# Kernel tuning notes

Measured on AMD Instinct MI355X. Metric: run time of the kernel, lower is better.

Reference implementation:

```python
import jax, jax.numpy as jnp
import numpy as np

EPS = 1e-7  # K.epsilon()
NUM_ROUTING = 3

def squash(v, axis=-1):
    s = jnp.sum(jnp.square(v), axis=axis, keepdims=True)
    scale = s / (1.0 + s) / jnp.sqrt(s + EPS)
    return scale * v

def setup_inputs() -> dict:
    key = jax.random.key(0)
    k1, k2 = jax.random.split(key)
    B, J, I = 64, 2048, 16   # batch, input_num_capsule, input_dim_capsule
    K_, D = 32, 16           # num_capsule, dim_capsule
    inputs = jax.random.normal(k1, (B, J, I), dtype=jnp.float32)
    W = jax.random.normal(k2, (K_, J, D, I), dtype=jnp.float32) * 0.05
    return {"inputs": inputs, "W": W}

def reference(inputs, W):
    # inputs: [B, J, I]; W: [K, J, D, I]
    # inputs_hat[b,k,j,d] = sum_i inputs[b,j,i] * W[k,j,d,i]
    u_hat = jnp.einsum('bji,kjdi->bkjd', inputs, W)  # [B,K,J,D]
    B, K_, J, D = u_hat.shape
    b = jnp.zeros((B, K_, J), dtype=u_hat.dtype)
    for i in range(NUM_ROUTING):
        c = jax.nn.softmax(b, axis=1)                # softmax over num_capsule (dim=1)
        s = jnp.einsum('bkj,bkjd->bkd', c, u_hat)    # [B,K,D]
        outputs = squash(s)
        if i < NUM_ROUTING - 1:
            b = b + jnp.einsum('bkd,bkjd->bkj', outputs, u_hat)
    return jnp.concatenate([outputs, c], axis=-1)    # [B, K, D+J]
```

## Files before the change

### kernel.cpp

```cpp
#include <hip/hip_runtime.h>
#include <hip/hip_bf16.h>

#define B_ 64
#define J_ 2048
#define K_ 32
#define D_ 16
#define KD 512
#define NCH 256
#define JCR 8

typedef __attribute__((ext_vector_type(8))) short short8v;
typedef __attribute__((ext_vector_type(16))) float f32x16;

__device__ __forceinline__ float bf2f(unsigned int bits16) {
  unsigned int u = bits16 << 16;
  return __builtin_bit_cast(float, u);
}
__device__ __forceinline__ unsigned int f2bf(float f) {
  unsigned int u = __builtin_bit_cast(unsigned int, f);
  u = u + 0x7fffu + ((u >> 16) & 1u);
  return u >> 16;
}
__device__ __forceinline__ unsigned int cvtpk(float lo, float hi) {
  unsigned int r;
  asm("v_cvt_pk_bf16_f32 %0, %1, %2" : "=v"(r) : "v"(lo), "v"(hi));
  return r;
}
__device__ __forceinline__ f32x16 zero16() {
  f32x16 z;
#pragma unroll
  for (int i = 0; i < 16; ++i) z[i] = 0.f;
  return z;
}

__global__ __launch_bounds__(256) void k_prepX(const float* __restrict__ inp,
                                               unsigned short* __restrict__ XT) {
  const size_t tid = (size_t)blockIdx.x * 256 + threadIdx.x;
  const size_t stride = (size_t)gridDim.x * 256;
  for (size_t g8 = tid; g8 < (size_t)J_ * B_ * 2; g8 += stride) {
    const size_t o = g8 * 8;
    const int j = (int)(o >> 10), b = (int)((o >> 4) & 63), i0 = (int)(o & 15);
    const float* src = inp + ((size_t)b * J_ + j) * 16 + i0;
    const float4 a = *(const float4*)src;
    const float4 c = *(const float4*)(src + 4);
    uint4 pk;
    pk.x = cvtpk(a.x, a.y);
    pk.y = cvtpk(a.z, a.w);
    pk.z = cvtpk(c.x, c.y);
    pk.w = cvtpk(c.z, c.w);
    *(uint4*)(XT + o) = pk;
  }
}

__global__ __launch_bounds__(512, 2) void k_R0W(const float* __restrict__ W,
                                                const unsigned short* __restrict__ XT,
                                                unsigned short* __restrict__ WB,
                                                unsigned int* __restrict__ spart_pk) {
  const int ch = blockIdx.x;
  const int t = threadIdx.x;
  const int wave = t >> 6, lane = t & 63;
  const int kq = wave & 3, bt = wave >> 2;
  const int hi = lane >> 5, b31 = lane & 31;
  const int b = bt * 32 + b31;
  const int j0 = ch * JCR;

  const float* wsrc = W + ((size_t)(8 * kq + (b31 >> 4)) * J_ + j0) * 256 +
                      (b31 & 15) * 16 + 8 * hi;
  unsigned short* wdst = WB + (size_t)j0 * 8192 + kq * 2048 + (b31 >> 4) * 256 +
                         (b31 & 15) * 16 + 8 * hi;
  const unsigned short* xBase = XT + (size_t)j0 * 1024 + b * 16 + 8 * hi;
  const size_t qstep = (size_t)2 * J_ * 256;

  f32x16 acc[4];
#pragma unroll
  for (int q = 0; q < 4; ++q) acc[q] = zero16();

  float4 wc[8];
  uint4 xc;
#pragma unroll
  for (int q = 0; q < 4; ++q) {
    wc[2 * q]     = *(const float4*)(wsrc + (size_t)q * qstep);
    wc[2 * q + 1] = *(const float4*)(wsrc + (size_t)q * qstep + 4);
  }
  xc = *(const uint4*)xBase;

  for (int jj = 0; jj < JCR; ++jj) {
    float4 wn[8];
    uint4 xn;
    if (jj + 1 < JCR) {
#pragma unroll
      for (int q = 0; q < 4; ++q) {
        const float* ws2 = wsrc + (size_t)(jj + 1) * 256 + (size_t)q * qstep;
        wn[2 * q] = *(const float4*)ws2;
        wn[2 * q + 1] = *(const float4*)(ws2 + 4);
      }
      xn = *(const uint4*)(xBase + (size_t)(jj + 1) * 1024);
    }
    const short8v xf = __builtin_bit_cast(short8v, xc);
#pragma unroll
    for (int q = 0; q < 4; ++q) {
      uint4 wv;
      wv.x = cvtpk(wc[2 * q].x, wc[2 * q].y);
      wv.y = cvtpk(wc[2 * q].z, wc[2 * q].w);
      wv.z = cvtpk(wc[2 * q + 1].x, wc[2 * q + 1].y);
      wv.w = cvtpk(wc[2 * q + 1].z, wc[2 * q + 1].w);
      if (bt == 0) *(uint4*)(wdst + (size_t)jj * 8192 + q * 512) = wv;
      acc[q] = __builtin_amdgcn_mfma_f32_32x32x16_bf16(
          __builtin_bit_cast(short8v, wv), xf, acc[q], 0, 0, 0);
    }
#pragma unroll
    for (int p = 0; p < 8; ++p) wc[p] = wn[p];
    xc = xn;
  }

  const float sc = 1.f / 32.f;
#pragma unroll
  for (int q = 0; q < 4; ++q) {
    const int keven = 8 * kq + 2 * q;
    unsigned int* se = spart_pk + (((size_t)b * NCH + ch) * 32 + keven) * 8 + 2 * hi;
    *(uint2*)se = make_uint2(cvtpk(acc[q][0] * sc, acc[q][1] * sc),
                             cvtpk(acc[q][2] * sc, acc[q][3] * sc));
    *(uint2*)(se + 4) = make_uint2(cvtpk(acc[q][4] * sc, acc[q][5] * sc),
                                   cvtpk(acc[q][6] * sc, acc[q][7] * sc));
    unsigned int* so = se + 8;
    *(uint2*)so = make_uint2(cvtpk(acc[q][8] * sc, acc[q][9] * sc),
                             cvtpk(acc[q][10] * sc, acc[q][11] * sc));
    *(uint2*)(so + 4) = make_uint2(cvtpk(acc[q][12] * sc, acc[q][13] * sc),
                                   cvtpk(acc[q][14] * sc, acc[q][15] * sc));
  }
}

template <int MODE>
__global__ __launch_bounds__(512, 2) void k_R(const unsigned short* __restrict__ XT,
                                              const unsigned short* __restrict__ WB,
                                              const unsigned short* __restrict__ osB,
                                              unsigned int* __restrict__ spart_pk,
                                              float* __restrict__ outp) {
  const int ch = blockIdx.x;
  const int t = threadIdx.x;
  const int wave = t >> 6, lane = t & 63;
  const int kq = wave & 3, bt = wave >> 2;
  const int hi = lane >> 5, b31 = lane & 31;
  const int b = bt * 32 + b31;
  const int j0 = ch * JCR;

  __shared__ float Sbuf[2 * 4 * 2 * 32];
  __shared__ float c_lds[(MODE == 2) ? 32 * 64 * 9 : 4];

  uint4 os_pk[8];
  {
    const unsigned short* osb = osB + ((size_t)bt * 64 + lane) * 8 + (size_t)(8 * kq) * 1024;
#pragma unroll
    for (int kk = 0; kk < 8; ++kk) os_pk[kk] = *(const uint4*)(osb + (size_t)kk * 1024);
  }

  float acc[4][16];
#pragma unroll
  for (int q = 0; q < 4; ++q)
#pragma unroll
    for (int s = 0; s < 16; ++s) acc[q][s] = 0.f;

  const unsigned short* waBase =
      WB + (size_t)j0 * 8192 + (b31 >> 4) * 256 + (b31 & 15) * 16 + 8 * hi + (size_t)kq * 2048;
  const unsigned short* xBase = XT + (size_t)j0 * 1024 + b * 16 + 8 * hi;

  uint4 a_cur[4], b_cur;
#pragma unroll
  for (int q = 0; q < 4; ++q) a_cur[q] = *(const uint4*)(waBase + q * 512);
  b_cur = *(const uint4*)(xBase);

  for (int jj = 0; jj < JCR; ++jj) {
    uint4 a_nxt[4], b_nxt;
    if (jj + 1 < JCR) {
#pragma unroll
      for (int q = 0; q < 4; ++q)
        a_nxt[q] = *(const uint4*)(waBase + (size_t)(jj + 1) * 8192 + q * 512);
      b_nxt = *(const uint4*)(xBase + (size_t)(jj + 1) * 1024);
    }

    f32x16 u[4];
#pragma unroll
    for (int q = 0; q < 4; ++q)
      u[q] = __builtin_amdgcn_mfma_f32_32x32x16_bf16(
          __builtin_bit_cast(short8v, a_cur[q]), __builtin_bit_cast(short8v, b_cur),
          zero16(), 0, 0, 0);

    float ee[4], eo[4];
    float Sp = 0.f;
#pragma unroll
    for (int q = 0; q < 4; ++q) {
      const unsigned int* o0 = (const unsigned int*)&os_pk[2 * q];
      const unsigned int* o1 = (const unsigned int*)&os_pk[2 * q + 1];
      float pe = 0.f, po = 0.f;
#pragma unroll
      for (int s = 0; s < 8; ++s) {
        const unsigned int w0 = o0[s >> 1], w1 = o1[s >> 1];
        pe = fmaf(u[q][s], bf2f((s & 1) ? (w0 >> 16) : (w0 & 0xffffu)), pe);
        po = fmaf(u[q][8 + s], bf2f((s & 1) ? (w1 >> 16) : (w1 & 0xffffu)), po);
      }
      pe += __shfl_xor(pe, 32);
      po += __shfl_xor(po, 32);
      ee[q] = __expf(pe);
      eo[q] = __expf(po);
      Sp += ee[q] + eo[q];
    }
    if (hi == 0) Sbuf[((jj & 1) * 8 + kq * 2 + bt) * 32 + b31] = Sp;
    __syncthreads();
    const int sb = (jj & 1) * 8;
    const float S = Sbuf[(sb + 0 * 2 + bt) * 32 + b31] + Sbuf[(sb + 1 * 2 + bt) * 32 + b31] +
                    Sbuf[(sb + 2 * 2 + bt) * 32 + b31] + Sbuf[(sb + 3 * 2 + bt) * 32 + b31];
    const float rS = __builtin_amdgcn_rcpf(S);
#pragma unroll
    for (int q = 0; q < 4; ++q) {
      const float ce = ee[q] * rS, co = eo[q] * rS;
#pragma unroll
      for (int s = 0; s < 8; ++s) {
        acc[q][s] = fmaf(ce, u[q][s], acc[q][s]);
        acc[q][8 + s] = fmaf(co, u[q][8 + s], acc[q][8 + s]);
      }
      if constexpr (MODE == 2) {
        if (hi == 0) {
          const int k0 = 8 * kq + 2 * q;
          c_lds[((k0)*64 + b) * 9 + jj] = ce;
          c_lds[((k0 + 1) * 64 + b) * 9 + jj] = co;
        }
      }
    }
#pragma unroll
    for (int q = 0; q < 4; ++q) a_cur[q] = a_nxt[q];
    b_cur = b_nxt;
  }

#pragma unroll
  for (int q = 0; q < 4; ++q) {
    const int keven = 8 * kq + 2 * q;
    unsigned int* se = spart_pk + (((size_t)b * NCH + ch) * 32 + keven) * 8 + 2 * hi;
    *(uint2*)se = make_uint2(cvtpk(acc[q][0], acc[q][1]), cvtpk(acc[q][2], acc[q][3]));
    *(uint2*)(se + 4) = make_uint2(cvtpk(acc[q][4], acc[q][5]), cvtpk(acc[q][6], acc[q][7]));
    unsigned int* so = se + 8;
    *(uint2*)so = make_uint2(cvtpk(acc[q][8], acc[q][9]), cvtpk(acc[q][10], acc[q][11]));
    *(uint2*)(so + 4) =
        make_uint2(cvtpk(acc[q][12], acc[q][13]), cvtpk(acc[q][14], acc[q][15]));
  }

  if constexpr (MODE == 2) {
    __syncthreads();
#pragma unroll
    for (int m = 0; m < 4; ++m) {
      const int r = m * 512 + t;
      const int k = r >> 6, bb = r & 63;
      const float* cr = &c_lds[r * 9];
      float* orow = outp + ((size_t)bb * K_ + k) * 2064 + 16 + j0;
      *(float4*)orow = make_float4(cr[0], cr[1], cr[2], cr[3]);
      *(float4*)(orow + 4) = make_float4(cr[4], cr[5], cr[6], cr[7]);
    }
  }
}

__global__ __launch_bounds__(256) void k_squash(const unsigned int* __restrict__ spart_pk,
                                                float* __restrict__ osum,
                                                unsigned short* __restrict__ osB,
                                                float* __restrict__ outp,
                                                int first, int final_) {
  const int t = threadIdx.x;
  const int wave = t >> 6, lane = t & 63;
  const int gw = blockIdx.x * 4 + wave;
  const int b = gw >> 5, k = gw & 31;
  const int h = lane & 7, pg = lane >> 3;
  float s0 = 0.f, s1 = 0.f;
#pragma unroll 8
  for (int p = pg; p < NCH; p += 8) {
    const unsigned int v = spart_pk[(((size_t)b * NCH + p) * 32 + k) * 8 + h];
    s0 += bf2f(v & 0xffffu);
    s1 += bf2f(v >> 16);
  }
  s0 += __shfl_xor(s0, 8);  s1 += __shfl_xor(s1, 8);
  s0 += __shfl_xor(s0, 16); s1 += __shfl_xor(s1, 16);
  s0 += __shfl_xor(s0, 32); s1 += __shfl_xor(s1, 32);
  float ss = s0 * s0 + s1 * s1;
  ss += __shfl_xor(ss, 1); ss += __shfl_xor(ss, 2); ss += __shfl_xor(ss, 4);
  const float scale = (ss / (1.f + ss)) * rsqrtf(ss + 1e-7f);
  const float ov0 = scale * s0, ov1 = scale * s1;
  if (final_) {
    if (pg == 0)
      *(float2*)(outp + ((size_t)b * K_ + k) * 2064 + 2 * h) = make_float2(ov0, ov1);
  } else {
    if (pg == 0) {
      float2 prev = make_float2(0.f, 0.f);
      if (!first) prev = *(const float2*)(osum + b * KD + k * 16 + 2 * h);
      const float ns0 = prev.x + ov0, ns1 = prev.y + ov1;
      *(float2*)(osum + b * KD + k * 16 + 2 * h) = make_float2(ns0, ns1);
      const int d0 = 2 * h;
      const int hi0 = (d0 >> 2) & 1;
      const int slot0 = (d0 & 3) + ((d0 >> 3) << 2);
      *(unsigned int*)(osB + (((size_t)k * 2 + (b >> 5)) * 64 + hi0 * 32 + (b & 31)) * 8 +
                       slot0) = cvtpk(ns0, ns1);
    }
  }
}

extern "C" void kernel_launch(void* const* d_in, const int* in_sizes, int n_in,
                              void* d_out, int out_size, void* d_ws, size_t ws_size,
                              hipStream_t stream) {
  const float* inp = (const float*)d_in[0];
  const float* W   = (const float*)d_in[1];
  float* outp = (float*)d_out;
  char* ws = (char*)d_ws;
  unsigned short* WB = (unsigned short*)ws;
  unsigned short* XT = (unsigned short*)(ws + (size_t)33554432);
  unsigned int* spart_pk = (unsigned int*)(ws + (size_t)37748736);
  float* osum  = (float*)(ws + (size_t)54525952);
  unsigned short* osB = (unsigned short*)(ws + (size_t)54525952 + 131072);

  k_prepX<<<512, 256, 0, stream>>>(inp, XT);
  k_R0W<<<NCH, 512, 0, stream>>>(W, XT, WB, spart_pk);
  k_squash<<<B_ * K_ / 4, 256, 0, stream>>>(spart_pk, osum, osB, outp, 1, 0);
  k_R<1><<<NCH, 512, 0, stream>>>(XT, WB, osB, spart_pk, nullptr);
  k_squash<<<B_ * K_ / 4, 256, 0, stream>>>(spart_pk, osum, osB, outp, 0, 0);
  k_R<2><<<NCH, 512, 0, stream>>>(XT, WB, osB, spart_pk, outp);
  k_squash<<<B_ * K_ / 4, 256, 0, stream>>>(spart_pk, osum, osB, outp, 0, 1);
}
```

Baseline: 93.49 us.

## Split k_R0W work by capsule across waves so W is loaded once per block

Each wave in k_R0W now owns four capsules and covers both 32-batch tiles, where before four waves each held eight capsules for a single batch tile. Every W element is therefore loaded from global memory and converted to bf16 once per block, not twice, and the WB store no longer needs a bt==0 guard. Each converted W fragment feeds two MFMAs, one per batch tile. Launch bounds for k_R0W and k_R drop from 2 to 1 block per CU, which frees registers but may lower occupancy.

Measured after the change: 84.83 us. 1.1x faster.

```diff
diff --git a/kernel.cpp b/kernel.cpp
--- a/kernel.cpp
+++ b/kernel.cpp
@@ -52,86 +52,93 @@
   }
 }
 
-__global__ __launch_bounds__(512, 2) void k_R0W(const float* __restrict__ W,
+__global__ __launch_bounds__(512, 1) void k_R0W(const float* __restrict__ W,
                                                 const unsigned short* __restrict__ XT,
                                                 unsigned short* __restrict__ WB,
                                                 unsigned int* __restrict__ spart_pk) {
   const int ch = blockIdx.x;
   const int t = threadIdx.x;
   const int wave = t >> 6, lane = t & 63;
-  const int kq = wave & 3, bt = wave >> 2;
   const int hi = lane >> 5, b31 = lane & 31;
-  const int b = bt * 32 + b31;
   const int j0 = ch * JCR;
 
-  const float* wsrc = W + ((size_t)(8 * kq + (b31 >> 4)) * J_ + j0) * 256 +
+  const float* wsrc = W + ((size_t)(4 * wave + (b31 >> 4)) * J_ + j0) * 256 +
                       (b31 & 15) * 16 + 8 * hi;
-  unsigned short* wdst = WB + (size_t)j0 * 8192 + kq * 2048 + (b31 >> 4) * 256 +
+  unsigned short* wdst = WB + (size_t)j0 * 8192 + (4 * wave + (b31 >> 4)) * 256 +
                          (b31 & 15) * 16 + 8 * hi;
-  const unsigned short* xBase = XT + (size_t)j0 * 1024 + b * 16 + 8 * hi;
+  const unsigned short* xBase = XT + (size_t)j0 * 1024 + b31 * 16 + 8 * hi;
   const size_t qstep = (size_t)2 * J_ * 256;
 
-  f32x16 acc[4];
-#pragma unroll
-  for (int q = 0; q < 4; ++q) acc[q] = zero16();
-
-  float4 wc[8];
-  uint4 xc;
-#pragma unroll
-  for (int q = 0; q < 4; ++q) {
+  f32x16 acc[2][2];
+#pragma unroll
+  for (int q = 0; q < 2; ++q)
+#pragma unroll
+    for (int bt = 0; bt < 2; ++bt) acc[q][bt] = zero16();
+
+  float4 wc[4];
+  uint4 xc[2];
+#pragma unroll
+  for (int q = 0; q < 2; ++q) {
     wc[2 * q]     = *(const float4*)(wsrc + (size_t)q * qstep);
     wc[2 * q + 1] = *(const float4*)(wsrc + (size_t)q * qstep + 4);
   }
-  xc = *(const uint4*)xBase;
+  xc[0] = *(const uint4*)(xBase);
+  xc[1] = *(const uint4*)(xBase + 512);
 
   for (int jj = 0; jj < JCR; ++jj) {
-    float4 wn[8];
-    uint4 xn;
+    float4 wn[4];
+    uint4 xn[2];
     if (jj + 1 < JCR) {
 #pragma unroll
-      for (int q = 0; q < 4; ++q) {
+      for (int q = 0; q < 2; ++q) {
         const float* ws2 = wsrc + (size_t)(jj + 1) * 256 + (size_t)q * qstep;
         wn[2 * q] = *(const float4*)ws2;
         wn[2 * q + 1] = *(const float4*)(ws2 + 4);
       }
-      xn = *(const uint4*)(xBase + (size_t)(jj + 1) * 1024);
-    }
-    const short8v xf = __builtin_bit_cast(short8v, xc);
-#pragma unroll
-    for (int q = 0; q < 4; ++q) {
+      xn[0] = *(const uint4*)(xBase + (size_t)(jj + 1) * 1024);
+      xn[1] = *(const uint4*)(xBase + (size_t)(jj + 1) * 1024 + 512);
+    }
+    const short8v xf0 = __builtin_bit_cast(short8v, xc[0]);
+    const short8v xf1 = __builtin_bit_cast(short8v, xc[1]);
+#pragma unroll
+    for (int q = 0; q < 2; ++q) {
       uint4 wv;
       wv.x = cvtpk(wc[2 * q].x, wc[2 * q].y);
       wv.y = cvtpk(wc[2 * q].z, wc[2 * q].w);
       wv.z = cvtpk(wc[2 * q + 1].x, wc[2 * q + 1].y);
       wv.w = cvtpk(wc[2 * q + 1].z, wc[2 * q + 1].w);
-      if (bt == 0) *(uint4*)(wdst + (size_t)jj * 8192 + q * 512) = wv;
-      acc[q] = __builtin_amdgcn_mfma_f32_32x32x16_bf16(
-          __builtin_bit_cast(short8v, wv), xf, acc[q], 0, 0, 0);
-    }
-#pragma unroll
-    for (int p = 0; p < 8; ++p) wc[p] = wn[p];
-    xc = xn;
+      *(uint4*)(wdst + (size_t)jj * 8192 + q * 512) = wv;
+      const short8v af = __builtin_bit_cast(short8v, wv);
+      acc[q][0] = __builtin_amdgcn_mfma_f32_32x32x16_bf16(af, xf0, acc[q][0], 0, 0, 0);
+      acc[q][1] = __builtin_amdgcn_mfma_f32_32x32x16_bf16(af, xf1, acc[q][1], 0, 0, 0);
+    }
+#pragma unroll
+    for (int p = 0; p < 4; ++p) wc[p] = wn[p];
+    xc[0] = xn[0];
+    xc[1] = xn[1];
   }
 
   const float sc = 1.f / 32.f;
 #pragma unroll
-  for (int q = 0; q < 4; ++q) {
-    const int keven = 8 * kq + 2 * q;
-    unsigned int* se = spart_pk + (((size_t)b * NCH + ch) * 32 + keven) * 8 + 2 * hi;
-    *(uint2*)se = make_uint2(cvtpk(acc[q][0] * sc, acc[q][1] * sc),
-                             cvtpk(acc[q][2] * sc, acc[q][3] * sc));
-    *(uint2*)(se + 4) = make_uint2(cvtpk(acc[q][4] * sc, acc[q][5] * sc),
-                                   cvtpk(acc[q][6] * sc, acc[q][7] * sc));
-    unsigned int* so = se + 8;
-    *(uint2*)so = make_uint2(cvtpk(acc[q][8] * sc, acc[q][9] * sc),
-                             cvtpk(acc[q][10] * sc, acc[q][11] * sc));
-    *(uint2*)(so + 4) = make_uint2(cvtpk(acc[q][12] * sc, acc[q][13] * sc),
-                                   cvtpk(acc[q][14] * sc, acc[q][15] * sc));
+  for (int q = 0; q < 2; ++q) {
+#pragma unroll
+    for (int bt = 0; bt < 2; ++bt) {
+      const int keven = 4 * wave + 2 * q;
+      const int b = bt * 32 + b31;
+      const float* a = (const float*)&acc[q][bt];
+      unsigned int* se = spart_pk + (((size_t)b * NCH + ch) * 32 + keven) * 8 + 2 * hi;
+      *(uint2*)se = make_uint2(cvtpk(a[0] * sc, a[1] * sc), cvtpk(a[2] * sc, a[3] * sc));
+      *(uint2*)(se + 4) = make_uint2(cvtpk(a[4] * sc, a[5] * sc), cvtpk(a[6] * sc, a[7] * sc));
+      unsigned int* so = se + 8;
+      *(uint2*)so = make_uint2(cvtpk(a[8] * sc, a[9] * sc), cvtpk(a[10] * sc, a[11] * sc));
+      *(uint2*)(so + 4) =
+          make_uint2(cvtpk(a[12] * sc, a[13] * sc), cvtpk(a[14] * sc, a[15] * sc));
+    }
   }
 }
 
 template <int MODE>
-__global__ __launch_bounds__(512, 2) void k_R(const unsigned short* __restrict__ XT,
+__global__ __launch_bounds__(512, 1) void k_R(const unsigned short* __restrict__ XT,
                                               const unsigned short* __restrict__ WB,
                                               const unsigned short* __restrict__ osB,
                                               unsigned int* __restrict__ spart_pk,
```
